# Performance work log

Measured on AMD Instinct MI355X. Metric: run time of the kernel, lower is better.

Reference implementation:

```python
import jax, jax.numpy as jnp
import numpy as np


def setup_inputs() -> dict:
    key = jax.random.key(0)
    k1, k2, k3 = jax.random.split(key, 3)
    dim, heads, dim_head, rows = 512, 8, 64, 64
    b, t = 4, 256
    _dim = heads * dim_head
    x = jax.random.normal(k1, (b * rows, t, dim), dtype=jnp.float32)
    # torch nn.Linear weight layout: [out_features, in_features]
    W_qkv = jax.random.normal(k2, (3 * _dim, dim), dtype=jnp.float32) * (dim ** -0.5)
    W0 = jax.random.normal(k3, (dim, _dim), dtype=jnp.float32) * (_dim ** -0.5)
    return {"x": x, "W_qkv": W_qkv, "W0": W0, "rows": rows, "heads": heads}


def reference(x, W_qkv, W0, rows, heads):
    br, t, dim = x.shape
    b = br // rows
    three_dim = W_qkv.shape[0]
    dim_head = three_dim // (3 * heads)
    scale = (rows * dim_head) ** -0.5

    qkv = x @ W_qkv.T  # [(b*rows), t, 3*heads*dim_head]
    # einops '(b rows) t (d k h) -> k b rows h t d': last dim ordered (d, k, h)
    qkv = qkv.reshape(b, rows, t, dim_head, 3, heads)
    qkv = jnp.transpose(qkv, (4, 0, 1, 5, 2, 3))  # [3, b, rows, h, t, d]
    q, k, v = qkv[0], qkv[1], qkv[2]

    # tied-row attention: sum QK^T over rows before a single shared softmax
    scores = jnp.einsum('brhid,brhjd->bhij', q, k) * scale  # [b, h, t, t]
    attn = jax.nn.softmax(scores, axis=-1)
    # broadcast shared attention map back across rows
    out = jnp.einsum('bhij,brhjd->brhid', attn, v)  # [b, rows, h, t, d]
    # 'b rows h t d -> (b rows) t (h d)'
    out = jnp.transpose(out, (0, 1, 3, 2, 4)).reshape(br, t, heads * dim_head)
    return out @ W0.T
```

## Files before the change

### kernel.cpp

```cpp
#include <hip/hip_runtime.h>


typedef short  bf16x8 __attribute__((ext_vector_type(8)));
typedef float  f32x4  __attribute__((ext_vector_type(4)));

#define MFMA16(a,b,c) __builtin_amdgcn_mfma_f32_16x16x32_bf16((a),(b),(c),0,0,0)

__device__ __forceinline__ ushort f2bf(float f) {
  union { float f; unsigned u; } v; v.f = f;
  unsigned r = v.u + 0x7fffu + ((v.u >> 16) & 1u);
  return (ushort)(r >> 16);
}

__device__ __forceinline__ void gload_lds16(const void* g, void* lds) {
  __builtin_amdgcn_global_load_lds(
      (const __attribute__((address_space(1))) void*)g,
      (__attribute__((address_space(3))) void*)lds, 16, 0, 0);
}


__global__ void prep_k(const float* __restrict__ W, ushort* __restrict__ Wp,
                       const float* __restrict__ W0, ushort* __restrict__ W0b) {
  const int bid = blockIdx.x, tid = threadIdx.x;
  if (bid < 768) {
    int np = (bid << 1) + (tid >> 7);
    int c  = tid & 127;
    int k = np >> 9, h = (np >> 6) & 7, d = np & 63;
    float4 f = reinterpret_cast<const float4*>(
        W + (size_t)(d * 24 + k * 8 + h) * 512)[c];
    ushort4 u; u.x = f2bf(f.x); u.y = f2bf(f.y); u.z = f2bf(f.z); u.w = f2bf(f.w);
    reinterpret_cast<ushort4*>(Wp + (size_t)np * 512)[c] = u;
  } else {
    int v0 = ((bid - 768) << 10) + (tid << 2);
#pragma unroll
    for (int q = 0; q < 4; ++q) {
      int v = v0 + q;
      float4 f = reinterpret_cast<const float4*>(W0)[v];
      ushort4 u; u.x = f2bf(f.x); u.y = f2bf(f.y); u.z = f2bf(f.z); u.w = f2bf(f.w);
      reinterpret_cast<ushort4*>(W0b)[v] = u;
    }
  }
}


__device__ __forceinline__ void gemm_nt_256x128(
    const ushort* __restrict__ A, const ushort* __restrict__ B,
    int lda, int ldb, int P, int m0, int n0, char* lds, f32x4 (&acc)[8][4]) {
  const int tid = threadIdx.x;
  const int w = tid >> 6, l = tid & 63;
  const int il = l & 15, kl = l >> 4;
  const int wm = w >> 1, wn = w & 1;

  auto stageA = [&](char* buf, int kt) {
#pragma unroll
    for (int c = 0; c < 4; ++c) {
      int rbase = (w << 6) + (c << 4);
      int row = rbase + (l >> 2);
      int s = ((l & 3) - ((row >> 1) & 3)) & 3;
      gload_lds16(A + (size_t)(m0 + row) * lda + (kt << 5) + (s << 3),
                  buf + rbase * 64);
    }
  };
  auto stageB = [&](char* buf, int kt) {
#pragma unroll
    for (int c = 0; c < 2; ++c) {
      int rbase = (w << 5) + (c << 4);
      int row = rbase + (l >> 2);
      int s = ((l & 3) - ((row >> 1) & 3)) & 3;
      gload_lds16(B + (size_t)(n0 + row) * ldb + (kt << 5) + (s << 3),
                  buf + 16384 + rbase * 64);
    }
  };
  auto loadA8 = [&](const char* buf, bf16x8 (&af)[8]) {
#pragma unroll
    for (int q = 0; q < 8; ++q) {
      int row = (wm << 7) + (q << 4) + il;
      af[q] = *(const bf16x8*)(buf + row * 64 + (((kl + (row >> 1)) & 3) << 4));
    }
  };
  auto loadB4 = [&](const char* buf, bf16x8 (&bfr)[4]) {
#pragma unroll
    for (int q = 0; q < 4; ++q) {
      int row = (wn << 6) + (q << 4) + il;
      bfr[q] = *(const bf16x8*)(buf + 16384 + row * 64 + (((kl + (row >> 1)) & 3) << 4));
    }
  };

#pragma unroll
  for (int i = 0; i < 8; ++i)
#pragma unroll
    for (int j = 0; j < 4; ++j) acc[i][j] = f32x4{0.f, 0.f, 0.f, 0.f};

  stageA(lds, 0);         stageB(lds, 0);
  stageA(lds + 24576, 1); stageB(lds + 24576, 1);
  asm volatile("s_waitcnt vmcnt(6)" ::: "memory");
  __builtin_amdgcn_s_barrier();

  int cur = 0, nx = 2;
  for (int g = 0; g < P; ++g) {
    char* cbuf = lds + cur * 24576;
    char* sbuf = lds + nx * 24576;
    bf16x8 af[8], bfr[4];
    loadA8(cbuf, af);
    loadB4(cbuf, bfr);
    if (g + 2 < P) { stageA(sbuf, g + 2); stageB(sbuf, g + 2); }
    __builtin_amdgcn_s_setprio(1);
#pragma unroll
    for (int fm = 0; fm < 8; ++fm)
#pragma unroll
      for (int fn = 0; fn < 4; ++fn)
        acc[fm][fn] = MFMA16(af[fm], bfr[fn], acc[fm][fn]);
    __builtin_amdgcn_s_setprio(0);
    if (g + 2 < P) asm volatile("s_waitcnt vmcnt(6)" ::: "memory");
    else           asm volatile("s_waitcnt vmcnt(0)" ::: "memory");
    __builtin_amdgcn_s_barrier();
    cur = (cur == 2) ? 0 : cur + 1;
    nx  = (nx  == 2) ? 0 : nx  + 1;
  }
}


__global__ __launch_bounds__(256, 2) void gemm_qkv_k(
    const float* __restrict__ x, const ushort* __restrict__ Wp,
    ushort* __restrict__ Qb, ushort* __restrict__ Kb, ushort* __restrict__ Vt) {
  __shared__ __align__(16) char lds_s[73728];
  char* lds = lds_s;
  f32x4 acc[8][4];
  const int Bid = blockIdx.x;
  const int xcd = Bid & 7, idx = Bid >> 3;
  const int nt = idx % 12, pl = idx / 12;
  const int m0 = ((pl << 3) + xcd) << 8;
  const int n0 = nt << 7;

  const int tid = threadIdx.x, w = tid >> 6, l = tid & 63;
  const int il = l & 15, kl = l >> 4;
  const int wm = w >> 1, wn = w & 1;

  float4 ar[8];
  auto loadAx = [&](int kt) {
#pragma unroll
    for (int rd = 0; rd < 8; ++rd) {
      int row = (rd << 5) + (w << 3) + (l >> 3);
      ar[rd] = *reinterpret_cast<const float4*>(
          x + (size_t)(m0 + row) * 512 + (kt << 5) + ((l & 7) << 2));
    }
  };
  auto writeA = [&](char* buf) {
#pragma unroll
    for (int rd = 0; rd < 8; ++rd) {
      int row = (rd << 5) + (w << 3) + (l >> 3);
      int c = l & 7;
      int slot = (((c >> 1) + (row >> 1)) & 3);
      ushort4 h;
      h.x = f2bf(ar[rd].x); h.y = f2bf(ar[rd].y);
      h.z = f2bf(ar[rd].z); h.w = f2bf(ar[rd].w);
      *reinterpret_cast<ushort4*>(buf + row * 64 + (slot << 4) + ((c & 1) << 3)) = h;
    }
  };
  auto stageB = [&](char* buf, int kt) {
#pragma unroll
    for (int c = 0; c < 2; ++c) {
      int rbase = (w << 5) + (c << 4);
      int row = rbase + (l >> 2);
      int s = ((l & 3) - ((row >> 1) & 3)) & 3;
      gload_lds16(Wp + (size_t)(n0 + row) * 512 + (kt << 5) + (s << 3),
                  buf + 16384 + rbase * 64);
    }
  };
  auto loadA8 = [&](const char* buf, bf16x8 (&af)[8]) {
#pragma unroll
    for (int q = 0; q < 8; ++q) {
      int row = (wm << 7) + (q << 4) + il;
      af[q] = *(const bf16x8*)(buf + row * 64 + (((kl + (row >> 1)) & 3) << 4));
    }
  };
  auto loadB4 = [&](const char* buf, bf16x8 (&bfr)[4]) {
#pragma unroll
    for (int q = 0; q < 4; ++q) {
      int row = (wn << 6) + (q << 4) + il;
      bfr[q] = *(const bf16x8*)(buf + 16384 + row * 64 + (((kl + (row >> 1)) & 3) << 4));
    }
  };

#pragma unroll
  for (int i = 0; i < 8; ++i)
#pragma unroll
    for (int j = 0; j < 4; ++j) acc[i][j] = f32x4{0.f, 0.f, 0.f, 0.f};

  loadAx(0);
  asm volatile("s_waitcnt vmcnt(0)" ::: "memory");
  writeA(lds);
  loadAx(1);
  stageB(lds, 0); stageB(lds + 24576, 1);
  asm volatile("s_waitcnt vmcnt(2)" ::: "memory");
  asm volatile("s_waitcnt lgkmcnt(0)" ::: "memory");
  __builtin_amdgcn_s_barrier();

  int cur = 0;
  for (int g = 0; g < 16; ++g) {
    int wn1 = (cur == 2) ? 0 : cur + 1;
    int nx2 = (wn1 == 2) ? 0 : wn1 + 1;
    if (g + 1 < 16) writeA(lds + wn1 * 24576);
    bf16x8 af[8], bfr[4];
    loadA8(lds + cur * 24576, af);
    loadB4(lds + cur * 24576, bfr);
    if (g + 2 < 16) { loadAx(g + 2); stageB(lds + nx2 * 24576, g + 2); }
    __builtin_amdgcn_s_setprio(1);
#pragma unroll
    for (int fm = 0; fm < 8; ++fm)
#pragma unroll
      for (int fn = 0; fn < 4; ++fn)
        acc[fm][fn] = MFMA16(af[fm], bfr[fn], acc[fm][fn]);
    __builtin_amdgcn_s_setprio(0);
    if (g + 2 < 16) asm volatile("s_waitcnt vmcnt(2)" ::: "memory");
    else            asm volatile("s_waitcnt vmcnt(0)" ::: "memory");
    asm volatile("s_waitcnt lgkmcnt(0)" ::: "memory");
    __builtin_amdgcn_s_barrier();
    cur = wn1;
  }

  const int kq = n0 >> 9;
  const int br = m0 >> 8, b = br >> 6, r = br & 63;
  if (kq < 2) {
    ushort* dstb = kq ? Kb : Qb;
#pragma unroll
    for (int fm = 0; fm < 8; ++fm)
#pragma unroll
      for (int fn = 0; fn < 4; ++fn) {
        int n = n0 + (wn << 6) + (fn << 4) + il;
        int h = (n >> 6) & 7, d = n & 63;
#pragma unroll
        for (int j = 0; j < 4; ++j) {
          int i = (wm << 7) + (fm << 4) + (kl << 2) + j;
          size_t dst = ((size_t)((((b << 3) + h) << 8) + i) << 12) + (r << 6) + d;
          dstb[dst] = f2bf(acc[fm][fn][j]);
        }
      }
  } else {
#pragma unroll
    for (int fm = 0; fm < 8; ++fm)
#pragma unroll
      for (int fn = 0; fn < 4; ++fn) {
        int n = n0 - 1024 + (wn << 6) + (fn << 4) + il;
        int h = n >> 6, d = n & 63;
        int i0 = (wm << 7) + (fm << 4) + (kl << 2);
        size_t dst = (((size_t)((((b << 3) + h) << 12)) + (r << 6) + d) << 8) + i0;
        ushort4 pk; pk.x = f2bf(acc[fm][fn][0]); pk.y = f2bf(acc[fm][fn][1]);
        pk.z = f2bf(acc[fm][fn][2]); pk.w = f2bf(acc[fm][fn][3]);
        *reinterpret_cast<ushort4*>(&Vt[dst]) = pk;
      }
  }
}


__global__ __launch_bounds__(256, 2) void gemm_out_k(
    const ushort* __restrict__ O2, const ushort* __restrict__ W0b,
    float* __restrict__ out) {
  __shared__ __align__(16) char lds[73728];
  f32x4 acc[8][4];
  const int Bid = blockIdx.x;
  const int xcd = Bid & 7, idx = Bid >> 3;
  const int nt = idx & 3, pl = idx >> 2;
  const int m0 = ((pl << 3) + xcd) << 8;
  const int n0 = nt << 7;
  gemm_nt_256x128(O2, W0b, 512, 512, 16, m0, n0, lds, acc);

  const int tid = threadIdx.x, w = tid >> 6, l = tid & 63;
  const int il = l & 15, kl = l >> 4;
  const int wm = w >> 1, wn = w & 1;
#pragma unroll
  for (int fm = 0; fm < 8; ++fm)
#pragma unroll
    for (int fn = 0; fn < 4; ++fn) {
      int n = n0 + (wn << 6) + (fn << 4) + il;
#pragma unroll
      for (int j = 0; j < 4; ++j) {
        int m = m0 + (wm << 7) + (fm << 4) + (kl << 2) + j;
        out[(size_t)m * 512 + n] = acc[fm][fn][j];
      }
    }
}


__global__ __launch_bounds__(256, 2) void gemm_s_k(
    const ushort* __restrict__ Qb, const ushort* __restrict__ Kb,
    float* __restrict__ Sp) {
  __shared__ __align__(16) char lds[73728];
  f32x4 acc[8][4];
  const int Bid = blockIdx.x;
  const int nt = Bid & 1, z = Bid >> 1;
  const int bh = z >> 2, ks = z & 3;
  const int n0 = nt << 7;
  const size_t base = ((size_t)bh << 20) + ((size_t)ks << 10);
  gemm_nt_256x128(Qb + base, Kb + base, 4096, 4096, 32, 0, n0, lds, acc);

  const int tid = threadIdx.x, w = tid >> 6, l = tid & 63;
  const int il = l & 15, kl = l >> 4;
  const int wm = w >> 1, wn = w & 1;
  float* o = Sp + ((size_t)z << 16);
#pragma unroll
  for (int fm = 0; fm < 8; ++fm)
#pragma unroll
    for (int fn = 0; fn < 4; ++fn) {
      int n = n0 + (wn << 6) + (fn << 4) + il;
#pragma unroll
      for (int j = 0; j < 4; ++j) {
        int m = (wm << 7) + (fm << 4) + (kl << 2) + j;
        o[(size_t)m * 256 + n] = acc[fm][fn][j];
      }
    }
}


__global__ void softmax_k(const float* __restrict__ Sp, ushort* __restrict__ Pb) {
  const int w = threadIdx.x >> 6, l = threadIdx.x & 63;
  const int row = (blockIdx.x << 2) + w;
  const int bh = row >> 8, i = row & 255;
  const float4* p0 = reinterpret_cast<const float4*>(
      Sp + (((size_t)bh << 2) << 16) + ((size_t)i << 8)) + l;
  float4 a = p0[0], b2 = p0[16384], c = p0[32768], d = p0[49152];
  const float scale = 0.015625f;
  float s0 = (a.x + b2.x + c.x + d.x) * scale;
  float s1 = (a.y + b2.y + c.y + d.y) * scale;
  float s2 = (a.z + b2.z + c.z + d.z) * scale;
  float s3 = (a.w + b2.w + c.w + d.w) * scale;
  float m = fmaxf(fmaxf(s0, s1), fmaxf(s2, s3));
#pragma unroll
  for (int d2 = 1; d2 < 64; d2 <<= 1) m = fmaxf(m, __shfl_xor(m, d2));
  float e0 = __expf(s0 - m), e1 = __expf(s1 - m);
  float e2 = __expf(s2 - m), e3 = __expf(s3 - m);
  float sum = e0 + e1 + e2 + e3;
#pragma unroll
  for (int d2 = 1; d2 < 64; d2 <<= 1) sum += __shfl_xor(sum, d2);
  float r = 1.0f / sum;
  ushort4 p; p.x = f2bf(e0 * r); p.y = f2bf(e1 * r);
  p.z = f2bf(e2 * r); p.w = f2bf(e3 * r);
  reinterpret_cast<ushort4*>(Pb + ((size_t)bh << 16) + ((size_t)i << 8))[l] = p;
}


__global__ __launch_bounds__(256, 2) void gemm_pv_k(
    const ushort* __restrict__ Vt, const ushort* __restrict__ Pb,
    ushort* __restrict__ O2) {
  __shared__ __align__(16) char lds[73728];
  f32x4 acc[8][4];
  const int Bid = blockIdx.x;
  const int xcd = Bid & 7, idx = Bid >> 3;
  const int sub = idx & 31, grp = idx >> 5;
  const int bh = (grp << 3) + xcd, b = bh >> 3, h = bh & 7;
  const int m0 = (sub >> 1) << 8;
  const int n0 = (sub & 1) << 7;
  gemm_nt_256x128(Vt + ((size_t)bh << 20), Pb + ((size_t)bh << 16),
                  256, 256, 8, m0, n0, lds, acc);

  const int tid = threadIdx.x, w = tid >> 6, l = tid & 63;
  const int il = l & 15, kl = l >> 4;
  const int wm = w >> 1, wn = w & 1;
#pragma unroll
  for (int fm = 0; fm < 8; ++fm) {
    int rd0 = m0 + (wm << 7) + (fm << 4) + (kl << 2);
    int r = rd0 >> 6, d0 = rd0 & 63;
#pragma unroll
    for (int fn = 0; fn < 4; ++fn) {
      int i = n0 + (wn << 6) + (fn << 4) + il;
      ushort4 pk; pk.x = f2bf(acc[fm][fn][0]); pk.y = f2bf(acc[fm][fn][1]);
      pk.z = f2bf(acc[fm][fn][2]); pk.w = f2bf(acc[fm][fn][3]);
      *reinterpret_cast<ushort4*>(
          O2 + ((size_t)((((b << 6) + r) << 8) + i) << 9) + (h << 6) + d0) = pk;
    }
  }
}


extern "C" void kernel_launch(void* const* d_in, const int* in_sizes, int n_in,
                              void* d_out, int out_size, void* d_ws, size_t ws_size,
                              hipStream_t stream) {
  const float* x    = (const float*)d_in[0];
  const float* Wqkv = (const float*)d_in[1];
  const float* W0   = (const float*)d_in[2];
  float* out = (float*)d_out;

  char* ws = (char*)d_ws;
  ushort* Wp  = (ushort*)(ws + 67108864);
  ushort* W0b = (ushort*)(ws + 68681728);
  ushort* Qb  = (ushort*)(ws + 69206016);
  ushort* Kb  = (ushort*)(ws + 136314880);
  ushort* Vt  = (ushort*)(ws + 203423744);
  if (ws_size < 270532608ull) return;

  prep_k<<<832, 256, 0, stream>>>(Wqkv, Wp, W0, W0b);

  gemm_qkv_k<<<3072, 256, 0, stream>>>(x, Wp, Qb, Kb, Vt);

  float*  Sp = (float*)ws;
  ushort* Pb = Qb;
  ushort* O2 = (ushort*)ws;

  gemm_s_k<<<256, 256, 0, stream>>>(Qb, Kb, Sp);
  softmax_k<<<2048, 256, 0, stream>>>(Sp, Pb);
  gemm_pv_k<<<1024, 256, 0, stream>>>(Vt, Pb, O2);

  gemm_out_k<<<1024, 256, 0, stream>>>(O2, W0b, out);
}
```

Before: 334.7 us.

## Pre-cast x to bf16, make QKV/out GEMMs persistent, store partial scores in bf16

Adds a separate kernel that casts x to bf16, so the QKV GEMM can stage A with direct global-to-LDS loads instead of register load, convert and LDS write. The QKV and output GEMMs become persistent-style: each block walks several M tiles (4 and 2) in one continuous pipelined K loop and flushes accumulators at tile boundaries, with fewer blocks launched. The partial score buffer is written as bf16 instead of fp32, and gemm_s_k gets an XCD-aware block mapping. This adds an extra pass over x and lowers the precision of the partial scores in exchange for less memory traffic and longer pipelines.

```diff
diff --git a/kernel.cpp b/kernel.cpp
--- a/kernel.cpp
+++ b/kernel.cpp
@@ -12,12 +12,28 @@
   return (ushort)(r >> 16);
 }
 
+__device__ __forceinline__ float bf2f(ushort u) {
+  union { unsigned u; float f; } v; v.u = ((unsigned)u) << 16;
+  return v.f;
+}
+
 __device__ __forceinline__ void gload_lds16(const void* g, void* lds) {
   __builtin_amdgcn_global_load_lds(
       (const __attribute__((address_space(1))) void*)g,
       (__attribute__((address_space(3))) void*)lds, 16, 0, 0);
 }
 
+
+__global__ void cast_f32_to_bf16(const float* __restrict__ in,
+                                 ushort* __restrict__ out, int n4) {
+  int idx = blockIdx.x * blockDim.x + threadIdx.x;
+  int stride = gridDim.x * blockDim.x;
+  for (int v = idx; v < n4; v += stride) {
+    float4 f = reinterpret_cast<const float4*>(in)[v];
+    ushort4 o; o.x = f2bf(f.x); o.y = f2bf(f.y); o.z = f2bf(f.z); o.w = f2bf(f.w);
+    reinterpret_cast<ushort4*>(out)[v] = o;
+  }
+}
 
 __global__ void prep_k(const float* __restrict__ W, ushort* __restrict__ Wp,
                        const float* __restrict__ W0, ushort* __restrict__ W0b) {
@@ -121,43 +137,37 @@
 
 
 __global__ __launch_bounds__(256, 2) void gemm_qkv_k(
-    const float* __restrict__ x, const ushort* __restrict__ Wp,
+    const ushort* __restrict__ xb, const ushort* __restrict__ Wp,
     ushort* __restrict__ Qb, ushort* __restrict__ Kb, ushort* __restrict__ Vt) {
   __shared__ __align__(16) char lds_s[73728];
   char* lds = lds_s;
   f32x4 acc[8][4];
   const int Bid = blockIdx.x;
   const int xcd = Bid & 7, idx = Bid >> 3;
-  const int nt = idx % 12, pl = idx / 12;
-  const int m0 = ((pl << 3) + xcd) << 8;
+  const int nt = idx % 12, pg = idx / 12;
   const int n0 = nt << 7;
+  const int kq = n0 >> 9;
 
   const int tid = threadIdx.x, w = tid >> 6, l = tid & 63;
   const int il = l & 15, kl = l >> 4;
   const int wm = w >> 1, wn = w & 1;
 
-  float4 ar[8];
-  auto loadAx = [&](int kt) {
-#pragma unroll
-    for (int rd = 0; rd < 8; ++rd) {
-      int row = (rd << 5) + (w << 3) + (l >> 3);
-      ar[rd] = *reinterpret_cast<const float4*>(
-          x + (size_t)(m0 + row) * 512 + (kt << 5) + ((l & 7) << 2));
-    }
-  };
-  auto writeA = [&](char* buf) {
-#pragma unroll
-    for (int rd = 0; rd < 8; ++rd) {
-      int row = (rd << 5) + (w << 3) + (l >> 3);
-      int c = l & 7;
-      int slot = (((c >> 1) + (row >> 1)) & 3);
-      ushort4 h;
-      h.x = f2bf(ar[rd].x); h.y = f2bf(ar[rd].y);
-      h.z = f2bf(ar[rd].z); h.w = f2bf(ar[rd].w);
-      *reinterpret_cast<ushort4*>(buf + row * 64 + (slot << 4) + ((c & 1) << 3)) = h;
-    }
-  };
-  auto stageB = [&](char* buf, int kt) {
+  auto mtile_of = [&](int j) { return (((pg << 2) + (j >> 4)) << 3) + xcd; };
+
+  auto stageA = [&](char* buf, int j) {
+    const size_t m0j = (size_t)mtile_of(j) << 8;
+    const int kt = j & 15;
+#pragma unroll
+    for (int c = 0; c < 4; ++c) {
+      int rbase = (w << 6) + (c << 4);
+      int row = rbase + (l >> 2);
+      int s = ((l & 3) - ((row >> 1) & 3)) & 3;
+      gload_lds16(xb + (m0j + row) * 512 + (kt << 5) + (s << 3),
+                  buf + rbase * 64);
+    }
+  };
+  auto stageB = [&](char* buf, int j) {
+    const int kt = j & 15;
 #pragma unroll
     for (int c = 0; c < 2; ++c) {
       int rbase = (w << 5) + (c << 4);
@@ -181,30 +191,65 @@
       bfr[q] = *(const bf16x8*)(buf + 16384 + row * 64 + (((kl + (row >> 1)) & 3) << 4));
     }
   };
+  auto flush = [&](int mt) {
+    const int b = mt >> 6, r = mt & 63;
+    if (kq < 2) {
+      ushort* dstb = kq ? Kb : Qb;
+#pragma unroll
+      for (int fm = 0; fm < 8; ++fm)
+#pragma unroll
+        for (int fn = 0; fn < 4; ++fn) {
+          int n = n0 + (wn << 6) + (fn << 4) + il;
+          int h = (n >> 6) & 7, d = n & 63;
+#pragma unroll
+          for (int j = 0; j < 4; ++j) {
+            int i = (wm << 7) + (fm << 4) + (kl << 2) + j;
+            size_t dst = ((size_t)((((b << 3) + h) << 8) + i) << 12) + (r << 6) + d;
+            dstb[dst] = f2bf(acc[fm][fn][j]);
+          }
+        }
+    } else {
+#pragma unroll
+      for (int fm = 0; fm < 8; ++fm)
+#pragma unroll
+        for (int fn = 0; fn < 4; ++fn) {
+          int n = n0 - 1024 + (wn << 6) + (fn << 4) + il;
+          int h = n >> 6, d = n & 63;
+          int i0 = (wm << 7) + (fm << 4) + (kl << 2);
+          size_t dst = (((size_t)((((b << 3) + h) << 12)) + (r << 6) + d) << 8) + i0;
+          ushort4 pk; pk.x = f2bf(acc[fm][fn][0]); pk.y = f2bf(acc[fm][fn][1]);
+          pk.z = f2bf(acc[fm][fn][2]); pk.w = f2bf(acc[fm][fn][3]);
+          *reinterpret_cast<ushort4*>(&Vt[dst]) = pk;
+        }
+    }
+  };
 
 #pragma unroll
   for (int i = 0; i < 8; ++i)
 #pragma unroll
     for (int j = 0; j < 4; ++j) acc[i][j] = f32x4{0.f, 0.f, 0.f, 0.f};
 
-  loadAx(0);
-  asm volatile("s_waitcnt vmcnt(0)" ::: "memory");
-  writeA(lds);
-  loadAx(1);
-  stageB(lds, 0); stageB(lds + 24576, 1);
-  asm volatile("s_waitcnt vmcnt(2)" ::: "memory");
-  asm volatile("s_waitcnt lgkmcnt(0)" ::: "memory");
+  stageA(lds, 0);         stageB(lds, 0);
+  stageA(lds + 24576, 1); stageB(lds + 24576, 1);
+  asm volatile("s_waitcnt vmcnt(6)" ::: "memory");
   __builtin_amdgcn_s_barrier();
 
-  int cur = 0;
-  for (int g = 0; g < 16; ++g) {
-    int wn1 = (cur == 2) ? 0 : cur + 1;
-    int nx2 = (wn1 == 2) ? 0 : wn1 + 1;
-    if (g + 1 < 16) writeA(lds + wn1 * 24576);
+  int cur = 0, nx = 2;
+  const int G = 64;
+  for (int g = 0; g < G; ++g) {
+    if (g > 0 && (g & 15) == 0) {
+      flush(mtile_of(g - 1));
+#pragma unroll
+      for (int i = 0; i < 8; ++i)
+#pragma unroll
+        for (int j = 0; j < 4; ++j) acc[i][j] = f32x4{0.f, 0.f, 0.f, 0.f};
+    }
+    char* cbuf = lds + cur * 24576;
+    char* sbuf = lds + nx * 24576;
     bf16x8 af[8], bfr[4];
-    loadA8(lds + cur * 24576, af);
-    loadB4(lds + cur * 24576, bfr);
-    if (g + 2 < 16) { loadAx(g + 2); stageB(lds + nx2 * 24576, g + 2); }
+    loadA8(cbuf, af);
+    loadB4(cbuf, bfr);
+    if (g + 2 < G) { stageA(sbuf, g + 2); stageB(sbuf, g + 2); }
     __builtin_amdgcn_s_setprio(1);
 #pragma unroll
     for (int fm = 0; fm < 8; ++fm)
@@ -212,62 +257,146 @@
       for (int fn = 0; fn < 4; ++fn)
         acc[fm][fn] = MFMA16(af[fm], bfr[fn], acc[fm][fn]);
     __builtin_amdgcn_s_setprio(0);
-    if (g + 2 < 16) asm volatile("s_waitcnt vmcnt(2)" ::: "memory");
-    else            asm volatile("s_waitcnt vmcnt(0)" ::: "memory");
-    asm volatile("s_waitcnt lgkmcnt(0)" ::: "memory");
+    if (g + 2 < G) asm volatile("s_waitcnt vmcnt(6)" ::: "memory");
+    else           asm volatile("s_waitcnt vmcnt(0)" ::: "memory");
     __builtin_amdgcn_s_barrier();
-    cur = wn1;
-  }
-
-  const int kq = n0 >> 9;
-  const int br = m0 >> 8, b = br >> 6, r = br & 63;
-  if (kq < 2) {
-    ushort* dstb = kq ? Kb : Qb;
-#pragma unroll
-    for (int fm = 0; fm < 8; ++fm)
-#pragma unroll
-      for (int fn = 0; fn < 4; ++fn) {
-        int n = n0 + (wn << 6) + (fn << 4) + il;
-        int h = (n >> 6) & 7, d = n & 63;
-#pragma unroll
-        for (int j = 0; j < 4; ++j) {
-          int i = (wm << 7) + (fm << 4) + (kl << 2) + j;
-          size_t dst = ((size_t)((((b << 3) + h) << 8) + i) << 12) + (r << 6) + d;
-          dstb[dst] = f2bf(acc[fm][fn][j]);
-        }
-      }
-  } else {
-#pragma unroll
-    for (int fm = 0; fm < 8; ++fm)
-#pragma unroll
-      for (int fn = 0; fn < 4; ++fn) {
-        int n = n0 - 1024 + (wn << 6) + (fn << 4) + il;
-        int h = n >> 6, d = n & 63;
-        int i0 = (wm << 7) + (fm << 4) + (kl << 2);
-        size_t dst = (((size_t)((((b << 3) + h) << 12)) + (r << 6) + d) << 8) + i0;
-        ushort4 pk; pk.x = f2bf(acc[fm][fn][0]); pk.y = f2bf(acc[fm][fn][1]);
-        pk.z = f2bf(acc[fm][fn][2]); pk.w = f2bf(acc[fm][fn][3]);
-        *reinterpret_cast<ushort4*>(&Vt[dst]) = pk;
-      }
-  }
+    cur = (cur == 2) ? 0 : cur + 1;
+    nx  = (nx  == 2) ? 0 : nx  + 1;
+  }
+  flush(mtile_of(G - 1));
 }
 
 
 __global__ __launch_bounds__(256, 2) void gemm_out_k(
     const ushort* __restrict__ O2, const ushort* __restrict__ W0b,
     float* __restrict__ out) {
+  __shared__ __align__(16) char lds_s[73728];
+  char* lds = lds_s;
+  f32x4 acc[8][4];
+  const int Bid = blockIdx.x;
+  const int xcd = Bid & 7, idx = Bid >> 3;
+  const int nt = idx & 3, pg = idx >> 2;
+  const int n0 = nt << 7;
+
+  const int tid = threadIdx.x, w = tid >> 6, l = tid & 63;
+  const int il = l & 15, kl = l >> 4;
+  const int wm = w >> 1, wn = w & 1;
+
+  auto mtile_of = [&](int j) { return (((pg << 1) + (j >> 4)) << 3) + xcd; };
+
+  auto stageA = [&](char* buf, int j) {
+    const size_t m0j = (size_t)mtile_of(j) << 8;
+    const int kt = j & 15;
+#pragma unroll
+    for (int c = 0; c < 4; ++c) {
+      int rbase = (w << 6) + (c << 4);
+      int row = rbase + (l >> 2);
+      int s = ((l & 3) - ((row >> 1) & 3)) & 3;
+      gload_lds16(O2 + (m0j + row) * 512 + (kt << 5) + (s << 3),
+                  buf + rbase * 64);
+    }
+  };
+  auto stageB = [&](char* buf, int j) {
+    const int kt = j & 15;
+#pragma unroll
+    for (int c = 0; c < 2; ++c) {
+      int rbase = (w << 5) + (c << 4);
+      int row = rbase + (l >> 2);
+      int s = ((l & 3) - ((row >> 1) & 3)) & 3;
+      gload_lds16(W0b + (size_t)(n0 + row) * 512 + (kt << 5) + (s << 3),
+                  buf + 16384 + rbase * 64);
+    }
+  };
+  auto loadA8 = [&](const char* buf, bf16x8 (&af)[8]) {
+#pragma unroll
+    for (int q = 0; q < 8; ++q) {
+      int row = (wm << 7) + (q << 4) + il;
+      af[q] = *(const bf16x8*)(buf + row * 64 + (((kl + (row >> 1)) & 3) << 4));
+    }
+  };
+  auto loadB4 = [&](const char* buf, bf16x8 (&bfr)[4]) {
+#pragma unroll
+    for (int q = 0; q < 4; ++q) {
+      int row = (wn << 6) + (q << 4) + il;
+      bfr[q] = *(const bf16x8*)(buf + 16384 + row * 64 + (((kl + (row >> 1)) & 3) << 4));
+    }
+  };
+  auto flush = [&](int mt) {
+    const int mbase = mt << 8;
+#pragma unroll
+    for (int fm = 0; fm < 8; ++fm)
+#pragma unroll
+      for (int fn = 0; fn < 4; ++fn) {
+        int n = n0 + (wn << 6) + (fn << 4) + il;
+#pragma unroll
+        for (int j = 0; j < 4; ++j) {
+          int m = mbase + (wm << 7) + (fm << 4) + (kl << 2) + j;
+          out[(size_t)m * 512 + n] = acc[fm][fn][j];
+        }
+      }
+  };
+
+#pragma unroll
+  for (int i = 0; i < 8; ++i)
+#pragma unroll
+    for (int j = 0; j < 4; ++j) acc[i][j] = f32x4{0.f, 0.f, 0.f, 0.f};
+
+  stageA(lds, 0);         stageB(lds, 0);
+  stageA(lds + 24576, 1); stageB(lds + 24576, 1);
+  asm volatile("s_waitcnt vmcnt(6)" ::: "memory");
+  __builtin_amdgcn_s_barrier();
+
+  int cur = 0, nx = 2;
+  const int G = 32;
+  for (int g = 0; g < G; ++g) {
+    if (g > 0 && (g & 15) == 0) {
+      flush(mtile_of(g - 1));
+#pragma unroll
+      for (int i = 0; i < 8; ++i)
+#pragma unroll
+        for (int j = 0; j < 4; ++j) acc[i][j] = f32x4{0.f, 0.f, 0.f, 0.f};
+    }
+    char* cbuf = lds + cur * 24576;
+    char* sbuf = lds + nx * 24576;
+    bf16x8 af[8], bfr[4];
+    loadA8(cbuf, af);
+    loadB4(cbuf, bfr);
+    if (g + 2 < G) { stageA(sbuf, g + 2); stageB(sbuf, g + 2); }
+    __builtin_amdgcn_s_setprio(1);
+#pragma unroll
+    for (int fm = 0; fm < 8; ++fm)
+#pragma unroll
+      for (int fn = 0; fn < 4; ++fn)
+        acc[fm][fn] = MFMA16(af[fm], bfr[fn], acc[fm][fn]);
+    __builtin_amdgcn_s_setprio(0);
+    if (g + 2 < G) asm volatile("s_waitcnt vmcnt(6)" ::: "memory");
+    else           asm volatile("s_waitcnt vmcnt(0)" ::: "memory");
+    __builtin_amdgcn_s_barrier();
+    cur = (cur == 2) ? 0 : cur + 1;
+    nx  = (nx  == 2) ? 0 : nx  + 1;
+  }
+  flush(mtile_of(G - 1));
+}
+
+
+__global__ __launch_bounds__(256, 2) void gemm_s_k(
+    const ushort* __restrict__ Qb, const ushort* __restrict__ Kb,
+    ushort* __restrict__ Spb) {
   __shared__ __align__(16) char lds[73728];
   f32x4 acc[8][4];
   const int Bid = blockIdx.x;
-  const int xcd = Bid & 7, idx = Bid >> 3;
-  const int nt = idx & 3, pl = idx >> 2;
-  const int m0 = ((pl << 3) + xcd) << 8;
+  const int xcd = Bid & 7, t = Bid >> 3;
+  const int j8 = t & 7, bh = ((t >> 3) << 3) + xcd;
+  const int ks = j8 >> 1, nt = j8 & 1;
+  const int z = (bh << 2) + ks;
   const int n0 = nt << 7;
-  gemm_nt_256x128(O2, W0b, 512, 512, 16, m0, n0, lds, acc);
+  const size_t base = ((size_t)bh << 20) + ((size_t)ks << 10);
+  gemm_nt_256x128(Qb + base, Kb + base, 4096, 4096, 32, 0, n0, lds, acc);
 
   const int tid = threadIdx.x, w = tid >> 6, l = tid & 63;
   const int il = l & 15, kl = l >> 4;
   const int wm = w >> 1, wn = w & 1;
+  ushort* o = Spb + ((size_t)z << 16);
 #pragma unroll
   for (int fm = 0; fm < 8; ++fm)
 #pragma unroll
@@ -275,55 +404,27 @@
       int n = n0 + (wn << 6) + (fn << 4) + il;
 #pragma unroll
       for (int j = 0; j < 4; ++j) {
-        int m = m0 + (wm << 7) + (fm << 4) + (kl << 2) + j;
-        out[(size_t)m * 512 + n] = acc[fm][fn][j];
+        int m = (wm << 7) + (fm << 4) + (kl << 2) + j;
+        o[(size_t)m * 256 + n] = f2bf(acc[fm][fn][j]);
       }
     }
 }
 
 
-__global__ __launch_bounds__(256, 2) void gemm_s_k(
-    const ushort* __restrict__ Qb, const ushort* __restrict__ Kb,
-    float* __restrict__ Sp) {
-  __shared__ __align__(16) char lds[73728];
-  f32x4 acc[8][4];
-  const int Bid = blockIdx.x;
-  const int nt = Bid & 1, z = Bid >> 1;
-  const int bh = z >> 2, ks = z & 3;
-  const int n0 = nt << 7;
-  const size_t base = ((size_t)bh << 20) + ((size_t)ks << 10);
-  gemm_nt_256x128(Qb + base, Kb + base, 4096, 4096, 32, 0, n0, lds, acc);
-
-  const int tid = threadIdx.x, w = tid >> 6, l = tid & 63;
-  const int il = l & 15, kl = l >> 4;
-  const int wm = w >> 1, wn = w & 1;
-  float* o = Sp + ((size_t)z << 16);
-#pragma unroll
-  for (int fm = 0; fm < 8; ++fm)
-#pragma unroll
-    for (int fn = 0; fn < 4; ++fn) {
-      int n = n0 + (wn << 6) + (fn << 4) + il;
-#pragma unroll
-      for (int j = 0; j < 4; ++j) {
-        int m = (wm << 7) + (fm << 4) + (kl << 2) + j;
-        o[(size_t)m * 256 + n] = acc[fm][fn][j];
-      }
-    }
-}
-
-
-__global__ void softmax_k(const float* __restrict__ Sp, ushort* __restrict__ Pb) {
+__global__ void softmax_k(const ushort* __restrict__ Spb, ushort* __restrict__ Pb) {
   const int w = threadIdx.x >> 6, l = threadIdx.x & 63;
   const int row = (blockIdx.x << 2) + w;
   const int bh = row >> 8, i = row & 255;
-  const float4* p0 = reinterpret_cast<const float4*>(
-      Sp + (((size_t)bh << 2) << 16) + ((size_t)i << 8)) + l;
-  float4 a = p0[0], b2 = p0[16384], c = p0[32768], d = p0[49152];
+  const ushort4* p0 = reinterpret_cast<const ushort4*>(
+      Spb + (((size_t)bh << 2) << 16) + ((size_t)i << 8)) + l;
+  float s0 = 0.f, s1 = 0.f, s2 = 0.f, s3 = 0.f;
+#pragma unroll
+  for (int ks = 0; ks < 4; ++ks) {
+    ushort4 a = p0[(size_t)ks * 16384];
+    s0 += bf2f(a.x); s1 += bf2f(a.y); s2 += bf2f(a.z); s3 += bf2f(a.w);
+  }
   const float scale = 0.015625f;
-  float s0 = (a.x + b2.x + c.x + d.x) * scale;
-  float s1 = (a.y + b2.y + c.y + d.y) * scale;
-  float s2 = (a.z + b2.z + c.z + d.z) * scale;
-  float s3 = (a.w + b2.w + c.w + d.w) * scale;
+  s0 *= scale; s1 *= scale; s2 *= scale; s3 *= scale;
   float m = fmaxf(fmaxf(s0, s1), fmaxf(s2, s3));
 #pragma unroll
   for (int d2 = 1; d2 < 64; d2 <<= 1) m = fmaxf(m, __shfl_xor(m, d2));
@@ -381,6 +482,7 @@
   float* out = (float*)d_out;
 
   char* ws = (char*)d_ws;
+  ushort* xb  = (ushort*)(ws);
   ushort* Wp  = (ushort*)(ws + 67108864);
   ushort* W0b = (ushort*)(ws + 68681728);
   ushort* Qb  = (ushort*)(ws + 69206016);
@@ -388,17 +490,18 @@
   ushort* Vt  = (ushort*)(ws + 203423744);
   if (ws_size < 270532608ull) return;
 
+  cast_f32_to_bf16<<<2048, 256, 0, stream>>>(x, xb, 8388608);
   prep_k<<<832, 256, 0, stream>>>(Wqkv, Wp, W0, W0b);
 
-  gemm_qkv_k<<<3072, 256, 0, stream>>>(x, Wp, Qb, Kb, Vt);
-
-  float*  Sp = (float*)ws;
-  ushort* Pb = Qb;
-  ushort* O2 = (ushort*)ws;
-
-  gemm_s_k<<<256, 256, 0, stream>>>(Qb, Kb, Sp);
-  softmax_k<<<2048, 256, 0, stream>>>(Sp, Pb);
+  gemm_qkv_k<<<768, 256, 0, stream>>>(xb, Wp, Qb, Kb, Vt);
+
+  ushort* Spb = xb;
+  ushort* Pb  = Qb;
+  ushort* O2  = xb;
+
+  gemm_s_k<<<256, 256, 0, stream>>>(Qb, Kb, Spb);
+  softmax_k<<<2048, 256, 0, stream>>>(Spb, Pb);
   gemm_pv_k<<<1024, 256, 0, stream>>>(Vt, Pb, O2);
 
-  gemm_out_k<<<1024, 256, 0, stream>>>(O2, W0b, out);
-}
+  gemm_out_k<<<512, 256, 0, stream>>>(O2, W0b, out);
+}
```

After: 528.2 us. 57.8% more time.
